# Kernel optimization log

Hardware: AMD Instinct MI355X
Metric: run time of the kernel (lower is better)

The kernel has to match this reference:

```python
import jax, jax.numpy as jnp
import numpy as np

THRESHOLD = 0.5
NEG_POS_RATIO = 3
ALPHA = 10.0


def cxcy_to_xy(c):
    return jnp.concatenate([c[..., :2] - c[..., 2:] / 2, c[..., :2] + c[..., 2:] / 2], axis=-1)


def xy_to_cxcy(xy):
    return jnp.concatenate([(xy[..., :2] + xy[..., 2:]) / 2, xy[..., 2:] - xy[..., :2]], axis=-1)


def encode(cxcy, anc):
    # SSD encoding with variances 0.1 / 0.2 expressed as /10 and *5
    return jnp.concatenate([
        (cxcy[..., :2] - anc[..., :2]) / (anc[..., 2:] / 10.0),
        jnp.log(cxcy[..., 2:] / anc[..., 2:]) * 5.0,
    ], axis=-1)


def jaccard(a, b):
    # a: [N,4] corner boxes, b: [P,4] corner boxes -> [N,P] IoU
    lt = jnp.maximum(a[:, None, :2], b[None, :, :2])
    rb = jnp.minimum(a[:, None, 2:], b[None, :, 2:])
    wh = jnp.clip(rb - lt, 0.0)
    inter = wh[..., 0] * wh[..., 1]
    area_a = (a[:, 2] - a[:, 0]) * (a[:, 3] - a[:, 1])
    area_b = (b[:, 2] - b[:, 0]) * (b[:, 3] - b[:, 1])
    return inter / (area_a[:, None] + area_b[None, :] - inter)


def _match(boxes, labels, corner_anchor, center_anchor):
    # boxes: [N_obj,4] corner, labels: [N_obj]
    n_obj = boxes.shape[0]
    iou = jaccard(boxes, corner_anchor)                 # [N_obj, P]
    obj_idx = jnp.argmax(iou, axis=1)                   # best prior per object
    iou = iou.at[jnp.arange(n_obj), obj_idx].set(1.0)   # force-match best prior
    positive = jnp.any(iou >= THRESHOLD, axis=0)        # [P]
    max_prior_idx = jnp.argmax(iou, axis=0)             # best object per prior
    true_cls = (labels[max_prior_idx] + 1) * positive.astype(jnp.int32)
    true_locs = encode(xy_to_cxcy(boxes[max_prior_idx]), center_anchor)
    return positive, true_cls, true_locs


def setup_inputs() -> dict:
    B, P, C, NOBJ = 32, 24564, 21, 24
    keys = jax.random.split(jax.random.key(0), 7)
    pred_cls = jax.random.normal(keys[0], (B, P, C), dtype=jnp.float32)
    pred_loc = jax.random.normal(keys[1], (B, P, 4), dtype=jnp.float32) * 0.1
    cxy = jax.random.uniform(keys[2], (B, NOBJ, 2), minval=0.2, maxval=0.8)
    wh = jax.random.uniform(keys[3], (B, NOBJ, 2), minval=0.05, maxval=0.3)
    gt_boxes = jnp.clip(jnp.concatenate([cxy - wh / 2, cxy + wh / 2], axis=-1), 0.0, 1.0)
    gt_labels = jax.random.randint(keys[4], (B, NOBJ), 0, C - 1, dtype=jnp.int32)
    a_cxy = jax.random.uniform(keys[5], (P, 2), minval=0.0, maxval=1.0)
    a_wh = jax.random.uniform(keys[6], (P, 2), minval=0.05, maxval=0.4)
    center_anchor = jnp.concatenate([a_cxy, a_wh], axis=-1)
    return {"pred_cls": pred_cls, "pred_loc": pred_loc, "gt_boxes": gt_boxes,
            "gt_labels": gt_labels, "center_anchor": center_anchor}


def reference(pred_cls, pred_loc, gt_boxes, gt_labels, center_anchor):
    B, P, C = pred_cls.shape
    corner_anchor = cxcy_to_xy(center_anchor)
    positive, true_cls, true_locs = jax.vmap(_match, in_axes=(0, 0, None, None))(
        gt_boxes, gt_labels, corner_anchor, center_anchor)

    n_pos = positive.sum(axis=1)                        # [B]
    n_pos_total = n_pos.sum().astype(pred_loc.dtype)

    # localization: L1 mean over positive priors (4 coords each)
    pos_f = positive[..., None].astype(pred_loc.dtype)
    loc_loss = (jnp.abs(pred_loc - true_locs) * pos_f).sum() / (n_pos_total * 4.0)

    # per-element cross entropy [B, P]
    logp = jax.nn.log_softmax(pred_cls, axis=-1)
    ce = -jnp.take_along_axis(logp, true_cls[..., None], axis=-1)[..., 0]

    conf_pos = (ce * positive.astype(ce.dtype)).sum()
    ce_neg = jnp.where(positive, 0.0, ce)
    ce_neg_sorted = jnp.sort(ce_neg, axis=1)[:, ::-1]   # descending
    ranks = jnp.arange(P)[None, :]
    hard_mask = (ranks < (NEG_POS_RATIO * n_pos)[:, None]).astype(ce.dtype)
    conf_neg = (ce_neg_sorted * hard_mask).sum()
    conf_loss = (conf_pos + conf_neg) / n_pos_total

    loc_loss = ALPHA * loc_loss
    total_loss = conf_loss + loc_loss
    return total_loss, (conf_loss, loc_loss)
```

## Files before the change

### kernel.cpp

```cpp
#include <hip/hip_runtime.h>
#include <stdint.h>

#define B 32
#define P 24564
#define NCLS 21
#define NOBJ 24
#define THRESH 0.5f
#define NBKT 2048
#define LCAP 5376

#define OFF_ACC     0
#define OFF_ARRV    32
#define OFF_NPOS    64
#define OFF_OBJBEST 192
#define INIT_BYTES  6336
#define OFF_HIST    6336
#define OFF_CENEG   268480

__device__ __forceinline__ unsigned long long umax64(unsigned long long a, unsigned long long b) {
    return a > b ? a : b;
}

__global__ __launch_bounds__(256) void k_objmax(
    const float* __restrict__ gt_boxes, const float* __restrict__ anchor,
    unsigned long long* __restrict__ obj_best, unsigned* __restrict__ hist) {
#pragma clang fp contract(off)
    int b = blockIdx.y;
    int j = blockIdx.x;
    int tid = threadIdx.x;
    if (tid < 128) hist[(blockIdx.y * 16 + blockIdx.x) * 128 + tid] = 0u;
    __shared__ float4 sbox[NOBJ];
    __shared__ unsigned long long sbest[NOBJ];
    if (tid < NOBJ) {
        const float* g = gt_boxes + (size_t)(b * NOBJ + tid) * 4;
        sbox[tid] = make_float4(g[0], g[1], g[2], g[3]);
        sbest[tid] = 0ull;
    }
    __syncthreads();
    unsigned long long best[NOBJ];
#pragma unroll
    for (int n = 0; n < NOBJ; n++) best[n] = 0ull;
    int pend = min(P, (j + 1) * 1536);
    for (int p = j * 1536 + tid; p < pend; p += 256) {
        float4 a = *(const float4*)(anchor + (size_t)p * 4);
        float ax0 = a.x - a.z * 0.5f, ay0 = a.y - a.w * 0.5f;
        float ax1 = a.x + a.z * 0.5f, ay1 = a.y + a.w * 0.5f;
        float area_a = (ax1 - ax0) * (ay1 - ay0);
        unsigned pk = ~(unsigned)p;
#pragma unroll
        for (int n = 0; n < NOBJ; n++) {
            float4 bx = sbox[n];
            float ltx = fmaxf(bx.x, ax0), lty = fmaxf(bx.y, ay0);
            float rbx = fminf(bx.z, ax1), rby = fminf(bx.w, ay1);
            float w = fmaxf(rbx - ltx, 0.f), h = fmaxf(rby - lty, 0.f);
            float inter = w * h;
            float area_o = (bx.z - bx.x) * (bx.w - bx.y);
            float iou = inter / (area_o + area_a - inter);
            unsigned long long key = ((unsigned long long)__float_as_uint(iou) << 32) | pk;
            best[n] = umax64(best[n], key);
        }
    }
#pragma unroll
    for (int n = 0; n < NOBJ; n++) {
        unsigned long long v = best[n];
        for (int off = 32; off > 0; off >>= 1) v = umax64(v, __shfl_down(v, off, 64));
        if ((tid & 63) == 0) atomicMax(&sbest[n], v);
    }
    __syncthreads();
    if (tid < NOBJ) atomicMax(&obj_best[b * NOBJ + tid], sbest[tid]);
}

__global__ __launch_bounds__(256, 2) void k_mainB(
    const float* __restrict__ pred_cls, const float* __restrict__ pred_loc,
    const float* __restrict__ gt_boxes, const int* __restrict__ gt_labels,
    const float* __restrict__ anchor, const unsigned long long* __restrict__ obj_best,
    float* __restrict__ ce_neg, unsigned* __restrict__ hist,
    int* __restrict__ n_pos, double* __restrict__ acc) {
#pragma clang fp contract(off)
    __shared__ float4 sbox[NOBJ];
    __shared__ int slab[NOBJ];
    __shared__ int sobj[NOBJ];
    __shared__ unsigned shist[NBKT];
    __shared__ float swf[8];
    __shared__ int swi[4];
    const int tid = threadIdx.x;
    const int b = blockIdx.x / 24;
    const int j = blockIdx.x % 24;

    for (int i = tid; i < NBKT; i += 256) shist[i] = 0u;
    if (tid < NOBJ) {
        const float* g = gt_boxes + (size_t)(b * NOBJ + tid) * 4;
        sbox[tid] = make_float4(g[0], g[1], g[2], g[3]);
        slab[tid] = gt_labels[b * NOBJ + tid];
        sobj[tid] = (int)(~(unsigned)(obj_best[b * NOBJ + tid] & 0xFFFFFFFFull));
    }
    __syncthreads();

    int p0 = j * 1024 + tid * 4;
    float lsum = 0.f, cpos = 0.f;
    int lnp = 0;
    if (p0 < P) {
        float4 xx[21];
        const float4* xp = (const float4*)(pred_cls + ((size_t)b * P + p0) * NCLS);
#pragma unroll
        for (int k = 0; k < 21; k++) xx[k] = xp[k];
        const float* arr = (const float*)xx;
        float4 anc4[4];
#pragma unroll
        for (int r = 0; r < 4; r++) anc4[r] = ((const float4*)anchor)[p0 + r];
        float4 cev;
        float* cevp = (float*)&cev;
#pragma unroll
        for (int r = 0; r < 4; r++) {
            int p = p0 + r;
            float4 a = anc4[r];
            float ax0 = a.x - a.z * 0.5f, ay0 = a.y - a.w * 0.5f;
            float ax1 = a.x + a.z * 0.5f, ay1 = a.y + a.w * 0.5f;
            float area_a = (ax1 - ax0) * (ay1 - ay0);
            float bv = -1.f;
            int bn = 0;
#pragma unroll
            for (int n = 0; n < NOBJ; n++) {
                float4 bx = sbox[n];
                float ltx = fmaxf(bx.x, ax0), lty = fmaxf(bx.y, ay0);
                float rbx = fminf(bx.z, ax1), rby = fminf(bx.w, ay1);
                float w = fmaxf(rbx - ltx, 0.f), h = fmaxf(rby - lty, 0.f);
                float inter = w * h;
                float area_o = (bx.z - bx.x) * (bx.w - bx.y);
                float iou = inter / (area_o + area_a - inter);
                if (p == sobj[n]) iou = 1.0f;
                if (iou > bv) { bv = iou; bn = n; }
            }
            int pos = (bv >= THRESH) ? 1 : 0;
            int cls = pos ? (slab[bn] + 1) : 0;
            const float* x = arr + r * 21;
            float m = x[0];
#pragma unroll
            for (int q = 1; q < NCLS; q++) m = fmaxf(m, x[q]);
            float s = 0.f;
#pragma unroll
            for (int q = 0; q < NCLS; q++) s += __expf(x[q] - m);
            float xc = x[0];
#pragma unroll
            for (int q = 1; q < NCLS; q++) xc = (cls == q) ? x[q] : xc;
            float ce = m + __logf(s) - xc;
            if (pos) {
                lnp++;
                cpos += ce;
                cevp[r] = 0.f;
                float4 bx = sbox[bn];
                float bcx = (bx.x + bx.z) * 0.5f, bcy = (bx.y + bx.w) * 0.5f;
                float bw = bx.z - bx.x, bh = bx.w - bx.y;
                float t0 = (bcx - a.x) / (a.z / 10.0f);
                float t1 = (bcy - a.y) / (a.w / 10.0f);
                float t2 = __logf(bw / a.z) * 5.0f;
                float t3 = __logf(bh / a.w) * 5.0f;
                float4 pl = *(const float4*)(pred_loc + ((size_t)b * P + p) * 4);
                lsum += fabsf(pl.x - t0) + fabsf(pl.y - t1) + fabsf(pl.z - t2) + fabsf(pl.w - t3);
            } else {
                cevp[r] = ce;
                unsigned bk = __float_as_uint(ce) >> 20;
                atomicAdd(&shist[bk > 2047u ? 2047u : bk], 1u);
            }
        }
        *(float4*)(ce_neg + (size_t)b * P + p0) = cev;
    }
    for (int off = 32; off > 0; off >>= 1) {
        lsum += __shfl_down(lsum, off, 64);
        cpos += __shfl_down(cpos, off, 64);
        lnp  += __shfl_down(lnp, off, 64);
    }
    if ((tid & 63) == 0) { swf[tid >> 6] = lsum; swf[4 + (tid >> 6)] = cpos; swi[tid >> 6] = lnp; }
    __syncthreads();
    if (tid == 0) {
        float ls = swf[0] + swf[1] + swf[2] + swf[3];
        float cs = swf[4] + swf[5] + swf[6] + swf[7];
        int np = swi[0] + swi[1] + swi[2] + swi[3];
        if (np) atomicAdd(&n_pos[b], np);
        atomicAdd(&acc[0], (double)ls);
        atomicAdd(&acc[1], (double)cs);
    }
    for (int i = tid; i < NBKT; i += 256) {
        unsigned c = shist[i];
        if (c) atomicAdd(&hist[b * NBKT + i], c);
    }
}

__global__ __launch_bounds__(256) void k_sel(
    const float* __restrict__ ce_neg, const unsigned* __restrict__ hist,
    const int* __restrict__ n_pos, double* __restrict__ acc,
    unsigned* __restrict__ arrv, float* __restrict__ out) {
    __shared__ unsigned shist[NBKT];
    __shared__ unsigned slist[LCAP];
    __shared__ int swi[4];
    __shared__ double swd[4];
    __shared__ int sscal[4];
    const int bb = blockIdx.x;
    const int tid = threadIdx.x;
    int K = n_pos[bb] * 3;
    if (K > P) K = P;
    if (K > 0) {
        unsigned* part = slist;
        unsigned* w64 = slist + 256;
        for (int i = tid; i < NBKT; i += 256) shist[i] = hist[bb * NBKT + i];
        __syncthreads();
        unsigned ps = 0;
#pragma unroll
        for (int q = 0; q < 8; q++) ps += shist[tid * 8 + q];
        part[tid] = ps;
        __syncthreads();
        if (tid < 64) w64[tid] = part[tid * 4] + part[tid * 4 + 1] + part[tid * 4 + 2] + part[tid * 4 + 3];
        __syncthreads();
        if (tid == 0) {
            unsigned c = 0;
            int g = 63;
            for (; g >= 0; g--) { if (c + w64[g] >= (unsigned)K) break; c += w64[g]; }
            int b0, Kp;
            if (g < 0) {
                b0 = 0;
                Kp = K - (int)(c - shist[0]);
            } else {
                int i = g * 4 + 3;
                for (;; i--) { if (c + part[i] >= (unsigned)K) break; c += part[i]; }
                int q = i * 8 + 7;
                for (;; q--) { if (c + shist[q] >= (unsigned)K) break; c += shist[q]; }
                b0 = q; Kp = K - (int)c;
            }
            sscal[0] = b0; sscal[1] = Kp; sscal[2] = 0;
        }
        __syncthreads();
        int b0 = sscal[0], Kp = sscal[1];
        const uint4* x4 = (const uint4*)(ce_neg + (size_t)bb * P);
        double s = 0.0;
        for (int i = tid; i < P / 4; i += 256) {
            uint4 v = x4[i];
            unsigned vv[4] = {v.x, v.y, v.z, v.w};
#pragma unroll
            for (int r = 0; r < 4; r++) {
                int bk = (int)(vv[r] >> 20);
                if (bk > b0) {
                    s += (double)__uint_as_float(vv[r]);
                } else if (bk == b0) {
                    int pos = atomicAdd(&sscal[2], 1);
                    if (pos < LCAP) slist[pos] = vv[r];
                }
            }
        }
        __syncthreads();
        int lcnt = sscal[2];
        bool useList = (lcnt <= LCAP);
        const unsigned* src = useList ? slist : (const unsigned*)(ce_neg + (size_t)bb * P);
        int n = useList ? lcnt : P;
        unsigned T = (unsigned)b0 << 20;
        if (Kp > 0) {
            for (int bit = 19; bit >= 0; bit--) {
                unsigned cand = T | (1u << bit);
                int cc = 0;
                for (int i = tid; i < n; i += 256) {
                    unsigned v = src[i];
                    if (!useList && (int)(v >> 20) != b0) continue;
                    cc += (v >= cand) ? 1 : 0;
                }
                for (int off = 32; off > 0; off >>= 1) cc += __shfl_down(cc, off, 64);
                if ((tid & 63) == 0) swi[tid >> 6] = cc;
                __syncthreads();
                int tot = swi[0] + swi[1] + swi[2] + swi[3];
                __syncthreads();
                if (tot >= Kp) T = cand;
            }
            int cgt = 0;
            for (int i = tid; i < n; i += 256) {
                unsigned v = src[i];
                if (!useList && (int)(v >> 20) != b0) continue;
                if (v > T) { cgt++; s += (double)__uint_as_float(v); }
            }
            for (int off = 32; off > 0; off >>= 1) cgt += __shfl_down(cgt, off, 64);
            if ((tid & 63) == 0) swi[tid >> 6] = cgt;
            __syncthreads();
            if (tid == 0) sscal[3] = swi[0] + swi[1] + swi[2] + swi[3];
            __syncthreads();
        }
        for (int off = 32; off > 0; off >>= 1) s += __shfl_down(s, off, 64);
        if ((tid & 63) == 0) swd[tid >> 6] = s;
        __syncthreads();
        if (tid == 0) {
            double tot = swd[0] + swd[1] + swd[2] + swd[3];
            if (Kp > 0) tot += (double)(Kp - sscal[3]) * (double)__uint_as_float(T);
            atomicAdd(&acc[2], tot);
        }
    }
    __syncthreads();
    if (tid == 0) {
        __threadfence();
        unsigned done = __hip_atomic_fetch_add(arrv, 1u, __ATOMIC_ACQ_REL, __HIP_MEMORY_SCOPE_AGENT);
        if (done == B - 1) {
            int npt = 0;
            for (int k = 0; k < B; k++)
                npt += __hip_atomic_load((int*)&n_pos[k], __ATOMIC_RELAXED, __HIP_MEMORY_SCOPE_AGENT);
            unsigned long long u0 = __hip_atomic_load((unsigned long long*)&acc[0],
                                                      __ATOMIC_RELAXED, __HIP_MEMORY_SCOPE_AGENT);
            unsigned long long u1 = __hip_atomic_load((unsigned long long*)&acc[1],
                                                      __ATOMIC_RELAXED, __HIP_MEMORY_SCOPE_AGENT);
            unsigned long long u2 = __hip_atomic_load((unsigned long long*)&acc[2],
                                                      __ATOMIC_RELAXED, __HIP_MEMORY_SCOPE_AGENT);
            double a0 = __longlong_as_double((long long)u0);
            double a1 = __longlong_as_double((long long)u1);
            double a2 = __longlong_as_double((long long)u2);
            double npf = (double)npt;
            float conf = (float)((a1 + a2) / npf);
            float loc = 10.0f * (float)(a0 / (npf * 4.0));
            out[0] = conf + loc;
            out[1] = conf;
            out[2] = loc;
        }
    }
}

extern "C" void kernel_launch(void* const* d_in, const int* in_sizes, int n_in,
                              void* d_out, int out_size, void* d_ws, size_t ws_size,
                              hipStream_t stream) {
    const float* pred_cls = (const float*)d_in[0];
    const float* pred_loc = (const float*)d_in[1];
    const float* gt_boxes = (const float*)d_in[2];
    const int*   gt_labels = (const int*)d_in[3];
    const float* anchor   = (const float*)d_in[4];
    float* out = (float*)d_out;
    char* ws = (char*)d_ws;
    double* acc = (double*)(ws + OFF_ACC);
    unsigned* arrv = (unsigned*)(ws + OFF_ARRV);
    int* n_pos = (int*)(ws + OFF_NPOS);
    unsigned long long* obj_best = (unsigned long long*)(ws + OFF_OBJBEST);
    unsigned* hist = (unsigned*)(ws + OFF_HIST);
    float* ce_neg = (float*)(ws + OFF_CENEG);

    hipMemsetAsync(ws, 0, INIT_BYTES, stream);
    k_objmax<<<dim3(16, B), 256, 0, stream>>>(gt_boxes, anchor, obj_best, hist);
    k_mainB<<<24 * B, 256, 0, stream>>>(pred_cls, pred_loc, gt_boxes, gt_labels, anchor,
                                        obj_best, ce_neg, hist, n_pos, acc);
    k_sel<<<B, 256, 0, stream>>>(ce_neg, hist, n_pos, acc, arrv, out);
}
```

Before: 202.9 us.

## Fuse selection into main kernel via last-block-per-batch and drop memset

Removes the separate selection kernel. The last block to finish each batch, found with a per-batch arrival counter, now does the hard-negative top-K selection inside the main kernel. The hipMemsetAsync is replaced by zeroing the header inside k_objmax, and the global atomicMax on obj_best becomes per-block partial writes that the main kernel reduces. The 20-step bitwise threshold search is replaced by a three-level radix histogram refinement (2048/2048/512 buckets) with a parallel suffix-scan bound finder. The trade-offs are more shared memory per block, which may lower occupancy (launch bounds no longer request 2 blocks), and the selection tail running on only 32 blocks at the end.

After: 374.7 us. 1.85x slower.

```diff
diff --git a/kernel.cpp b/kernel.cpp
--- a/kernel.cpp
+++ b/kernel.cpp
@@ -7,37 +7,40 @@
 #define NOBJ 24
 #define THRESH 0.5f
 #define NBKT 2048
-#define LCAP 5376
-
-#define OFF_ACC     0
-#define OFF_ARRV    32
-#define OFF_NPOS    64
-#define OFF_OBJBEST 192
-#define INIT_BYTES  6336
-#define OFF_HIST    6336
-#define OFF_CENEG   268480
-
-__device__ __forceinline__ unsigned long long umax64(unsigned long long a, unsigned long long b) {
-    return a > b ? a : b;
-}
+#define LCAP 2816
+
+#define OFF_ACC      0
+#define OFF_ARRVALL  24
+#define OFF_BARRV    32
+#define OFF_NPOS     160
+#define HDR_WORDS    72
+#define OFF_OBJPART  288
+#define OFF_HIST     98592
+#define OFF_CENEG    360736
+
+typedef unsigned long long u64;
+__device__ __forceinline__ u64 umax64(u64 a, u64 b) { return a > b ? a : b; }
 
 __global__ __launch_bounds__(256) void k_objmax(
     const float* __restrict__ gt_boxes, const float* __restrict__ anchor,
-    unsigned long long* __restrict__ obj_best, unsigned* __restrict__ hist) {
+    char* __restrict__ ws) {
 #pragma clang fp contract(off)
     int b = blockIdx.y;
     int j = blockIdx.x;
     int tid = threadIdx.x;
-    if (tid < 128) hist[(blockIdx.y * 16 + blockIdx.x) * 128 + tid] = 0u;
+    unsigned* hist = (unsigned*)(ws + OFF_HIST);
+    u64* part = (u64*)(ws + OFF_OBJPART);
+    if (tid < 128) hist[(b * 16 + j) * 128 + tid] = 0u;
+    if (b == 0 && j == 0 && tid < HDR_WORDS) ((unsigned*)ws)[tid] = 0u;
     __shared__ float4 sbox[NOBJ];
-    __shared__ unsigned long long sbest[NOBJ];
+    __shared__ u64 sbest[NOBJ];
     if (tid < NOBJ) {
         const float* g = gt_boxes + (size_t)(b * NOBJ + tid) * 4;
         sbox[tid] = make_float4(g[0], g[1], g[2], g[3]);
         sbest[tid] = 0ull;
     }
     __syncthreads();
-    unsigned long long best[NOBJ];
+    u64 best[NOBJ];
 #pragma unroll
     for (int n = 0; n < NOBJ; n++) best[n] = 0ull;
     int pend = min(P, (j + 1) * 1536);
@@ -56,33 +59,83 @@
             float inter = w * h;
             float area_o = (bx.z - bx.x) * (bx.w - bx.y);
             float iou = inter / (area_o + area_a - inter);
-            unsigned long long key = ((unsigned long long)__float_as_uint(iou) << 32) | pk;
+            u64 key = ((u64)__float_as_uint(iou) << 32) | pk;
             best[n] = umax64(best[n], key);
         }
     }
 #pragma unroll
     for (int n = 0; n < NOBJ; n++) {
-        unsigned long long v = best[n];
+        u64 v = best[n];
         for (int off = 32; off > 0; off >>= 1) v = umax64(v, __shfl_down(v, off, 64));
         if ((tid & 63) == 0) atomicMax(&sbest[n], v);
     }
     __syncthreads();
-    if (tid < NOBJ) atomicMax(&obj_best[b * NOBJ + tid], sbest[tid]);
+    if (tid < NOBJ) part[((size_t)b * NOBJ + tid) * 16 + j] = sbest[tid];
 }
 
-__global__ __launch_bounds__(256, 2) void k_mainB(
+__device__ __forceinline__ void find_bound(const unsigned* shist, int NB, int K,
+                                           int* sscal, unsigned* wsum, int tid) {
+    int G = NB >> 8;
+    unsigned loc[8];
+    unsigned tot = 0;
+    for (int g = 0; g < G; g++) { loc[g] = shist[tid * G + g]; tot += loc[g]; }
+    unsigned v = tot;
+    int lane = tid & 63;
+    for (int off = 1; off < 64; off <<= 1) {
+        unsigned o = __shfl_down(v, off, 64);
+        if (lane + off < 64) v += o;
+    }
+    if (lane == 0) wsum[tid >> 6] = v;
+    __syncthreads();
+    unsigned above = 0;
+    for (int w = (tid >> 6) + 1; w < 4; w++) above += wsum[w];
+    unsigned sfx_excl = above + (v - tot);
+    unsigned snext = 0, sloc = 0;
+    for (int k = G - 1; k >= 0; k--) {
+        sloc = snext + loc[k];
+        unsigned sfx_i = sloc + sfx_excl;
+        unsigned sfx_n = snext + sfx_excl;
+        if (sfx_i >= (unsigned)K && sfx_n < (unsigned)K) {
+            sscal[0] = tid * G + k;
+            sscal[1] = K - (int)sfx_n;
+        }
+        snext = sloc;
+    }
+    if (tid == 0) {
+        unsigned total = sloc + sfx_excl;
+        if (total < (unsigned)K) {
+            sscal[0] = 0;
+            sscal[1] = K - (int)((sloc - loc[0]) + sfx_excl);
+        }
+    }
+    __syncthreads();
+}
+
+__global__ __launch_bounds__(256) void k_fused(
     const float* __restrict__ pred_cls, const float* __restrict__ pred_loc,
     const float* __restrict__ gt_boxes, const int* __restrict__ gt_labels,
-    const float* __restrict__ anchor, const unsigned long long* __restrict__ obj_best,
-    float* __restrict__ ce_neg, unsigned* __restrict__ hist,
-    int* __restrict__ n_pos, double* __restrict__ acc) {
+    const float* __restrict__ anchor, char* __restrict__ ws, float* __restrict__ out) {
 #pragma clang fp contract(off)
+    double* acc = (double*)(ws + OFF_ACC);
+    unsigned* arrv_all = (unsigned*)(ws + OFF_ARRVALL);
+    unsigned* batch_arrv = (unsigned*)(ws + OFF_BARRV);
+    int* n_pos = (int*)(ws + OFF_NPOS);
+    const u64* objpart = (const u64*)(ws + OFF_OBJPART);
+    unsigned* hist = (unsigned*)(ws + OFF_HIST);
+    float* ce_neg = (float*)(ws + OFF_CENEG);
+
     __shared__ float4 sbox[NOBJ];
     __shared__ int slab[NOBJ];
     __shared__ int sobj[NOBJ];
     __shared__ unsigned shist[NBKT];
+    __shared__ unsigned slist[LCAP];
+    __shared__ unsigned list2[LCAP];
     __shared__ float swf[8];
     __shared__ int swi[4];
+    __shared__ double swd[4];
+    __shared__ unsigned wsum[4];
+    __shared__ int sscal[4];
+
     const int tid = threadIdx.x;
     const int b = blockIdx.x / 24;
     const int j = blockIdx.x % 24;
@@ -92,7 +145,11 @@
         const float* g = gt_boxes + (size_t)(b * NOBJ + tid) * 4;
         sbox[tid] = make_float4(g[0], g[1], g[2], g[3]);
         slab[tid] = gt_labels[b * NOBJ + tid];
-        sobj[tid] = (int)(~(unsigned)(obj_best[b * NOBJ + tid] & 0xFFFFFFFFull));
+        const u64* pp = objpart + ((size_t)b * NOBJ + tid) * 16;
+        u64 m = pp[0];
+#pragma unroll
+        for (int q = 1; q < 16; q++) m = umax64(m, pp[q]);
+        sobj[tid] = (int)(~(unsigned)(m & 0xFFFFFFFFull));
     }
     __syncthreads();
 
@@ -158,9 +215,9 @@
                 float4 pl = *(const float4*)(pred_loc + ((size_t)b * P + p) * 4);
                 lsum += fabsf(pl.x - t0) + fabsf(pl.y - t1) + fabsf(pl.z - t2) + fabsf(pl.w - t3);
             } else {
-                cevp[r] = ce;
-                unsigned bk = __float_as_uint(ce) >> 20;
-                atomicAdd(&shist[bk > 2047u ? 2047u : bk], 1u);
+                float cen = fmaxf(ce, 0.f);
+                cevp[r] = cen;
+                atomicAdd(&shist[__float_as_uint(cen) >> 20], 1u);
             }
         }
         *(float4*)(ce_neg + (size_t)b * P + p0) = cev;
@@ -184,63 +241,39 @@
         unsigned c = shist[i];
         if (c) atomicAdd(&hist[b * NBKT + i], c);
     }
-}
-
-__global__ __launch_bounds__(256) void k_sel(
-    const float* __restrict__ ce_neg, const unsigned* __restrict__ hist,
-    const int* __restrict__ n_pos, double* __restrict__ acc,
-    unsigned* __restrict__ arrv, float* __restrict__ out) {
-    __shared__ unsigned shist[NBKT];
-    __shared__ unsigned slist[LCAP];
-    __shared__ int swi[4];
-    __shared__ double swd[4];
-    __shared__ int sscal[4];
-    const int bb = blockIdx.x;
-    const int tid = threadIdx.x;
-    int K = n_pos[bb] * 3;
+
+    __syncthreads();
+    if (tid == 0) {
+        __threadfence();
+        unsigned old = __hip_atomic_fetch_add(&batch_arrv[b], 1u,
+                                              __ATOMIC_ACQ_REL, __HIP_MEMORY_SCOPE_AGENT);
+        swi[0] = (old == 23) ? 1 : 0;
+    }
+    __syncthreads();
+    if (swi[0] == 0) return;
+
+    int npb = __hip_atomic_load(&n_pos[b], __ATOMIC_RELAXED, __HIP_MEMORY_SCOPE_AGENT);
+    int K = npb * 3;
     if (K > P) K = P;
+    double s = 0.0;
     if (K > 0) {
-        unsigned* part = slist;
-        unsigned* w64 = slist + 256;
-        for (int i = tid; i < NBKT; i += 256) shist[i] = hist[bb * NBKT + i];
+        for (int i = tid; i < NBKT; i += 256)
+            shist[i] = __hip_atomic_load(&hist[b * NBKT + i],
+                                         __ATOMIC_RELAXED, __HIP_MEMORY_SCOPE_AGENT);
         __syncthreads();
-        unsigned ps = 0;
-#pragma unroll
-        for (int q = 0; q < 8; q++) ps += shist[tid * 8 + q];
-        part[tid] = ps;
+        find_bound(shist, NBKT, K, sscal, wsum, tid);
+        int b0 = sscal[0], Kp0 = sscal[1];
+        if (tid == 0) sscal[2] = 0;
         __syncthreads();
-        if (tid < 64) w64[tid] = part[tid * 4] + part[tid * 4 + 1] + part[tid * 4 + 2] + part[tid * 4 + 3];
-        __syncthreads();
-        if (tid == 0) {
-            unsigned c = 0;
-            int g = 63;
-            for (; g >= 0; g--) { if (c + w64[g] >= (unsigned)K) break; c += w64[g]; }
-            int b0, Kp;
-            if (g < 0) {
-                b0 = 0;
-                Kp = K - (int)(c - shist[0]);
-            } else {
-                int i = g * 4 + 3;
-                for (;; i--) { if (c + part[i] >= (unsigned)K) break; c += part[i]; }
-                int q = i * 8 + 7;
-                for (;; q--) { if (c + shist[q] >= (unsigned)K) break; c += shist[q]; }
-                b0 = q; Kp = K - (int)c;
-            }
-            sscal[0] = b0; sscal[1] = Kp; sscal[2] = 0;
-        }
-        __syncthreads();
-        int b0 = sscal[0], Kp = sscal[1];
-        const uint4* x4 = (const uint4*)(ce_neg + (size_t)bb * P);
-        double s = 0.0;
+        const uint4* x4 = (const uint4*)(ce_neg + (size_t)b * P);
         for (int i = tid; i < P / 4; i += 256) {
             uint4 v = x4[i];
             unsigned vv[4] = {v.x, v.y, v.z, v.w};
 #pragma unroll
             for (int r = 0; r < 4; r++) {
                 int bk = (int)(vv[r] >> 20);
-                if (bk > b0) {
-                    s += (double)__uint_as_float(vv[r]);
-                } else if (bk == b0) {
+                if (bk > b0) s += (double)__uint_as_float(vv[r]);
+                else if (bk == b0) {
                     int pos = atomicAdd(&sscal[2], 1);
                     if (pos < LCAP) slist[pos] = vv[r];
                 }
@@ -248,61 +281,88 @@
         }
         __syncthreads();
         int lcnt = sscal[2];
-        bool useList = (lcnt <= LCAP);
-        const unsigned* src = useList ? slist : (const unsigned*)(ce_neg + (size_t)bb * P);
-        int n = useList ? lcnt : P;
-        unsigned T = (unsigned)b0 << 20;
-        if (Kp > 0) {
-            for (int bit = 19; bit >= 0; bit--) {
-                unsigned cand = T | (1u << bit);
-                int cc = 0;
-                for (int i = tid; i < n; i += 256) {
+        if (Kp0 > 0) {
+            if (lcnt <= LCAP) {
+                for (int i = tid; i < NBKT; i += 256) shist[i] = 0u;
+                __syncthreads();
+                for (int i = tid; i < lcnt; i += 256)
+                    atomicAdd(&shist[(slist[i] >> 9) & 0x7FFu], 1u);
+                __syncthreads();
+                find_bound(shist, NBKT, Kp0, sscal, wsum, tid);
+                int b1 = sscal[0], Kp1 = sscal[1];
+                if (tid == 0) sscal[3] = 0;
+                __syncthreads();
+                for (int i = tid; i < lcnt; i += 256) {
+                    unsigned v = slist[i];
+                    int sb = (int)((v >> 9) & 0x7FFu);
+                    if (sb > b1) s += (double)__uint_as_float(v);
+                    else if (sb == b1) list2[atomicAdd(&sscal[3], 1)] = v;
+                }
+                __syncthreads();
+                int n2 = sscal[3];
+                for (int i = tid; i < 512; i += 256) shist[i] = 0u;
+                __syncthreads();
+                for (int i = tid; i < n2; i += 256)
+                    atomicAdd(&shist[list2[i] & 0x1FFu], 1u);
+                __syncthreads();
+                find_bound(shist, 512, Kp1, sscal, wsum, tid);
+                int b2 = sscal[0], R = sscal[1];
+                for (int i = tid; i < n2; i += 256) {
+                    unsigned v = list2[i];
+                    if ((int)(v & 0x1FFu) > b2) s += (double)__uint_as_float(v);
+                }
+                unsigned Tbits = ((unsigned)b0 << 20) | ((unsigned)b1 << 9) | (unsigned)b2;
+                if (tid == 0) s += (double)R * (double)__uint_as_float(Tbits);
+            } else {
+                const unsigned* src = (const unsigned*)(ce_neg + (size_t)b * P);
+                unsigned T = (unsigned)b0 << 20;
+                for (int bit = 19; bit >= 0; bit--) {
+                    unsigned cand = T | (1u << bit);
+                    int cc = 0;
+                    for (int i = tid; i < P; i += 256) {
+                        unsigned v = src[i];
+                        if ((int)(v >> 20) == b0 && v >= cand) cc++;
+                    }
+                    for (int off = 32; off > 0; off >>= 1) cc += __shfl_down(cc, off, 64);
+                    if ((tid & 63) == 0) swi[tid >> 6] = cc;
+                    __syncthreads();
+                    int tot = swi[0] + swi[1] + swi[2] + swi[3];
+                    __syncthreads();
+                    if (tot >= Kp0) T = cand;
+                }
+                int cgt = 0;
+                for (int i = tid; i < P; i += 256) {
                     unsigned v = src[i];
-                    if (!useList && (int)(v >> 20) != b0) continue;
-                    cc += (v >= cand) ? 1 : 0;
-                }
-                for (int off = 32; off > 0; off >>= 1) cc += __shfl_down(cc, off, 64);
-                if ((tid & 63) == 0) swi[tid >> 6] = cc;
-                __syncthreads();
-                int tot = swi[0] + swi[1] + swi[2] + swi[3];
-                __syncthreads();
-                if (tot >= Kp) T = cand;
+                    if ((int)(v >> 20) == b0 && v > T) { cgt++; s += (double)__uint_as_float(v); }
+                }
+                for (int off = 32; off > 0; off >>= 1) cgt += __shfl_down(cgt, off, 64);
+                if ((tid & 63) == 0) swi[tid >> 6] = cgt;
+                __syncthreads();
+                if (tid == 0) {
+                    int cg = swi[0] + swi[1] + swi[2] + swi[3];
+                    s += (double)(Kp0 - cg) * (double)__uint_as_float(T);
+                }
+                __syncthreads();
             }
-            int cgt = 0;
-            for (int i = tid; i < n; i += 256) {
-                unsigned v = src[i];
-                if (!useList && (int)(v >> 20) != b0) continue;
-                if (v > T) { cgt++; s += (double)__uint_as_float(v); }
-            }
-            for (int off = 32; off > 0; off >>= 1) cgt += __shfl_down(cgt, off, 64);
-            if ((tid & 63) == 0) swi[tid >> 6] = cgt;
-            __syncthreads();
-            if (tid == 0) sscal[3] = swi[0] + swi[1] + swi[2] + swi[3];
-            __syncthreads();
         }
         for (int off = 32; off > 0; off >>= 1) s += __shfl_down(s, off, 64);
         if ((tid & 63) == 0) swd[tid >> 6] = s;
         __syncthreads();
-        if (tid == 0) {
-            double tot = swd[0] + swd[1] + swd[2] + swd[3];
-            if (Kp > 0) tot += (double)(Kp - sscal[3]) * (double)__uint_as_float(T);
-            atomicAdd(&acc[2], tot);
-        }
-    }
+        if (tid == 0) atomicAdd(&acc[2], swd[0] + swd[1] + swd[2] + swd[3]);
+    }
+
     __syncthreads();
     if (tid == 0) {
         __threadfence();
-        unsigned done = __hip_atomic_fetch_add(arrv, 1u, __ATOMIC_ACQ_REL, __HIP_MEMORY_SCOPE_AGENT);
-        if (done == B - 1) {
+        unsigned old = __hip_atomic_fetch_add(arrv_all, 1u,
+                                              __ATOMIC_ACQ_REL, __HIP_MEMORY_SCOPE_AGENT);
+        if (old == B - 1) {
             int npt = 0;
             for (int k = 0; k < B; k++)
-                npt += __hip_atomic_load((int*)&n_pos[k], __ATOMIC_RELAXED, __HIP_MEMORY_SCOPE_AGENT);
-            unsigned long long u0 = __hip_atomic_load((unsigned long long*)&acc[0],
-                                                      __ATOMIC_RELAXED, __HIP_MEMORY_SCOPE_AGENT);
-            unsigned long long u1 = __hip_atomic_load((unsigned long long*)&acc[1],
-                                                      __ATOMIC_RELAXED, __HIP_MEMORY_SCOPE_AGENT);
-            unsigned long long u2 = __hip_atomic_load((unsigned long long*)&acc[2],
-                                                      __ATOMIC_RELAXED, __HIP_MEMORY_SCOPE_AGENT);
+                npt += __hip_atomic_load(&n_pos[k], __ATOMIC_RELAXED, __HIP_MEMORY_SCOPE_AGENT);
+            u64 u0 = __hip_atomic_load((u64*)&acc[0], __ATOMIC_RELAXED, __HIP_MEMORY_SCOPE_AGENT);
+            u64 u1 = __hip_atomic_load((u64*)&acc[1], __ATOMIC_RELAXED, __HIP_MEMORY_SCOPE_AGENT);
+            u64 u2 = __hip_atomic_load((u64*)&acc[2], __ATOMIC_RELAXED, __HIP_MEMORY_SCOPE_AGENT);
             double a0 = __longlong_as_double((long long)u0);
             double a1 = __longlong_as_double((long long)u1);
             double a2 = __longlong_as_double((long long)u2);
@@ -326,16 +386,8 @@
     const float* anchor   = (const float*)d_in[4];
     float* out = (float*)d_out;
     char* ws = (char*)d_ws;
-    double* acc = (double*)(ws + OFF_ACC);
-    unsigned* arrv = (unsigned*)(ws + OFF_ARRV);
-    int* n_pos = (int*)(ws + OFF_NPOS);
-    unsigned long long* obj_best = (unsigned long long*)(ws + OFF_OBJBEST);
-    unsigned* hist = (unsigned*)(ws + OFF_HIST);
-    float* ce_neg = (float*)(ws + OFF_CENEG);
-
-    hipMemsetAsync(ws, 0, INIT_BYTES, stream);
-    k_objmax<<<dim3(16, B), 256, 0, stream>>>(gt_boxes, anchor, obj_best, hist);
-    k_mainB<<<24 * B, 256, 0, stream>>>(pred_cls, pred_loc, gt_boxes, gt_labels, anchor,
-                                        obj_best, ce_neg, hist, n_pos, acc);
-    k_sel<<<B, 256, 0, stream>>>(ce_neg, hist, n_pos, acc, arrv, out);
+
+    k_objmax<<<dim3(16, B), 256, 0, stream>>>(gt_boxes, anchor, ws);
+    k_fused<<<24 * B, 256, 0, stream>>>(pred_cls, pred_loc, gt_boxes, gt_labels,
+                                        anchor, ws, out);
 }
```
